# Optimization experiments

Hardware: AMD Instinct MI355X
Metric: run time of the kernel (lower is better)

The kernel has to match this reference:

```python
import jax, jax.numpy as jnp
import numpy as np
from jax import lax

# Hyperparameters from unifiedloss(__init__ defaults / init_kwargs)
WEIGHT = 1.0
DELTA = 0.6
GAMMA = 0.5
LABEL_SMOOTHING = 0.1
OUT_CHANNELS = 2
ALPHA = 0.9  # border_uncertainty inner-border weight
BETA = 0.9   # border_uncertainty outer-border weight
EPS = 1e-7


def _morph_3x3(x, is_dilate):
    # Binary morphology with a 3x3 ones structuring element == max/min pool.
    # x: [B, C, H, W]. 'SAME' padding with the reduction identity matches
    # ignoring out-of-image pixels.
    if is_dilate:
        return lax.reduce_window(x, -jnp.inf, lax.max, (1, 1, 3, 3), (1, 1, 1, 1), 'SAME')
    return lax.reduce_window(x, jnp.inf, lax.min, (1, 1, 3, 3), (1, 1, 1, 1), 'SAME')


def setup_inputs() -> dict:
    key = jax.random.key(0)
    k1, k2 = jax.random.split(key)
    B, C, H, W = 8, 2, 1024, 1024
    pred = jax.random.normal(k1, (B, C, H, W), dtype=jnp.float32)
    # one-hot binary ground truth (channel 0 = background, channel 1 = foreground)
    labels = jax.random.randint(k2, (B, H, W), 0, 2)
    target = jax.nn.one_hot(labels, C, dtype=jnp.float32).transpose(0, 3, 1, 2)
    return {"pred": pred, "target": target}


def reference(pred, target):
    # --- boundary uncertainty (vectorized over batch; all-zero samples give
    # erode = dilate = 0 so res = 0, matching the original early-return) ---
    im_erode = _morph_3x3(target, False)
    im_dilate = _morph_3x3(target, True)
    t = ALPHA * (target - im_erode) + BETA * (im_dilate - target) + im_erode

    # --- label smoothing ---
    t = t * (1.0 - LABEL_SMOOTHING) + LABEL_SMOOTHING / OUT_CHANNELS

    # --- valid-pixel mask: channel sum == 1 (only clean one-hot pixels kept) ---
    mf = (jnp.sum(t, axis=1) == 1.0).astype(pred.dtype)  # [B, H, W]
    n = jnp.sum(mf)

    p = jnp.clip(jax.nn.sigmoid(pred), EPS, 1.0 - EPS)  # [B, C, H, W]

    # --- asymmetric focal Tversky loss (masked per-class sums) ---
    tp = jnp.einsum('bhw,bchw->c', mf, t * p)
    fn = jnp.einsum('bhw,bchw->c', mf, t * (1.0 - p))
    fp = jnp.einsum('bhw,bchw->c', mf, (1.0 - t) * p)
    dice = (tp + EPS) / (tp + DELTA * fn + (1.0 - DELTA) * fp + EPS)
    back_dice = 1.0 - dice[0]
    fore_dice = (1.0 - dice[1]) * (1.0 - dice[1]) ** (-GAMMA)
    ftl = (back_dice + fore_dice) * 0.5

    # --- asymmetric focal loss (masked mean over pixels) ---
    ce = -t * jnp.log(p)  # [B, C, H, W]
    back_ce = (1.0 - DELTA) * (1.0 - p[:, 0]) ** GAMMA * ce[:, 0]
    fore_ce = DELTA * ce[:, 1]
    fl = jnp.sum(mf * (back_ce + fore_ce)) / n

    return WEIGHT * ftl + (1.0 - WEIGHT) * fl
```

## Files before the change

kernel.cpp:

```cpp
#include <hip/hip_runtime.h>
#include <math.h>

#define HH 1024
#define WW 1024
#define NB 8
#define ROWS 8
#define SW 256
#define STRIPES (WW / SW)
#define CHUNKS (HH / ROWS)
#define WPB (STRIPES * CHUNKS)
#define TOTAL_WAVES (NB * WPB)
#define NBLK (TOTAL_WAVES / 4)

__global__ __launch_bounds__(256) void ul_main(const float* __restrict__ pred,
                                               const float* __restrict__ target,
                                               float* __restrict__ partials) {
    const int wv   = threadIdx.x >> 6;
    const int lane = threadIdx.x & 63;
    const int wid  = (blockIdx.x << 2) | wv;
    const int b      = wid >> 9;
    const int rem    = wid & 511;
    const int stripe = rem & 3;
    const int chunk  = rem >> 2;
    const int c0     = stripe * SW;
    const int r0     = chunk * ROWS;
    const int col4   = c0 + lane * 4;

    const float* __restrict__ t1p = target + (size_t)(2 * b + 1) * (HH * WW);
    const float* __restrict__ p0p = pred   + (size_t)(2 * b)     * (HH * WW);
    const float* __restrict__ p1p = p0p + (size_t)HH * WW;

    const int excL = (c0 > 0) ? (c0 - 1) : 0;
    const int excR = (c0 + SW < WW) ? (c0 + SW) : (WW - 1);
    const int exc  = (lane == 0) ? excL : excR;

    float4 vm[ROWS + 2];
    unsigned ebPack = 0;
    #pragma unroll
    for (int i = 0; i < ROWS + 2; ++i) {
        int h = r0 - 1 + i;
        h = h < 0 ? 0 : (h >= HH ? HH - 1 : h);
        const float* rp = t1p + (size_t)h * WW;
        vm[i] = *(const float4*)(rp + col4);
        float ev = (lane < 2) ? rp[exc] : 0.0f;
        ebPack |= (ev > 0.5f ? 1u : 0u) << i;
    }
    const unsigned ebR = __shfl(ebPack, 1);

    unsigned pbits[ROWS + 2], w6[ROWS + 2];
    #pragma unroll
    for (int i = 0; i < ROWS + 2; ++i) {
        unsigned p = (vm[i].x > 0.5f ? 1u : 0u) | (vm[i].y > 0.5f ? 2u : 0u) |
                     (vm[i].z > 0.5f ? 4u : 0u) | (vm[i].w > 0.5f ? 8u : 0u);
        pbits[i] = p;
        const unsigned pl = __shfl_up(p, 1);
        const unsigned pr = __shfl_down(p, 1);
        const unsigned lb = (lane == 0)  ? ((ebPack >> i) & 1u) : ((pl >> 3) & 1u);
        const unsigned rb = (lane == 63) ? ((ebR    >> i) & 1u) : (pr & 1u);
        w6[i] = lb | (p << 1) | (rb << 5);
    }

    unsigned unis[ROWS];
    #pragma unroll
    for (int j = 0; j < ROWS; ++j) {
        const unsigned A = w6[j] & w6[j + 1] & w6[j + 2];
        const unsigned O = w6[j] | w6[j + 1] | w6[j + 2];
        const unsigned all1 = A & (A >> 1) & (A >> 2);
        const unsigned any1 = O | (O >> 1) | (O >> 2);
        unis[j] = (all1 | ~any1) & 0xFu;
    }

    float4 x0[ROWS], x1[ROWS];
    #pragma unroll
    for (int j = 0; j < ROWS; ++j) {
        if (unis[j]) {
            const size_t off = (size_t)(r0 + j) * WW + col4;
            x0[j] = *(const float4*)(p0p + off);
            x1[j] = *(const float4*)(p1p + off);
        }
    }

    float s_p0 = 0.f, s_lp0 = 0.f, s_p1 = 0.f, s_lp1 = 0.f;
    int nC = 0, nL = 0;
    #pragma unroll
    for (int j = 0; j < ROWS; ++j) {
        const unsigned uni = unis[j];
        if (uni) {
            const unsigned lb4 = pbits[j + 1];
            nC += __popc(uni);
            nL += __popc(uni & lb4);
            #define UL_DO_K(K, C0, C1)                                          \
                if ((uni >> K) & 1u) {                                          \
                    float sg0 = 1.0f / (1.0f + expf(-(C0)));                    \
                    float sg1 = 1.0f / (1.0f + expf(-(C1)));                    \
                    sg0 = fminf(fmaxf(sg0, 1e-7f), 1.0f - 1e-7f);               \
                    sg1 = fminf(fmaxf(sg1, 1e-7f), 1.0f - 1e-7f);               \
                    s_p0 += sg0; s_p1 += sg1;                                   \
                    if ((lb4 >> K) & 1u) { s_lp0 += sg0; s_lp1 += sg1; }        \
                }
            UL_DO_K(0, x0[j].x, x1[j].x)
            UL_DO_K(1, x0[j].y, x1[j].y)
            UL_DO_K(2, x0[j].z, x1[j].z)
            UL_DO_K(3, x0[j].w, x1[j].w)
            #undef UL_DO_K
        }
    }

    #pragma unroll
    for (int off = 32; off; off >>= 1) {
        s_p0  += __shfl_xor(s_p0,  off, 64);
        s_lp0 += __shfl_xor(s_lp0, off, 64);
        s_p1  += __shfl_xor(s_p1,  off, 64);
        s_lp1 += __shfl_xor(s_lp1, off, 64);
        nC    += __shfl_xor(nC,    off, 64);
        nL    += __shfl_xor(nL,    off, 64);
    }

    __shared__ float sm[4][6];
    if (lane == 0) {
        sm[wv][0] = s_p0;  sm[wv][1] = s_lp0;
        sm[wv][2] = s_p1;  sm[wv][3] = s_lp1;
        sm[wv][4] = (float)nC; sm[wv][5] = (float)nL;
    }
    __syncthreads();
    if (threadIdx.x < 8) {
        const int k = threadIdx.x;
        const float v = (k < 6) ? (sm[0][k] + sm[1][k] + sm[2][k] + sm[3][k]) : 0.0f;
        partials[(size_t)blockIdx.x * 8 + k] = v;
    }
}

__global__ __launch_bounds__(256) void ul_final(const float* __restrict__ ws,
                                                float* __restrict__ out) {
    const int t = threadIdx.x, lane = t & 63, wv = t >> 6;
    float a0 = 0.f, a1 = 0.f, a2 = 0.f, a3 = 0.f;
    #pragma unroll
    for (int r = 0; r < 8; ++r) {
        const float4 v = ((const float4*)ws)[t + 256 * r];
        a0 += v.x; a1 += v.y; a2 += v.z; a3 += v.w;
    }
    #pragma unroll
    for (int off = 32; off >= 2; off >>= 1) {
        a0 += __shfl_xor(a0, off, 64); a1 += __shfl_xor(a1, off, 64);
        a2 += __shfl_xor(a2, off, 64); a3 += __shfl_xor(a3, off, 64);
    }
    __shared__ float sm[4][2][4];
    if (lane < 2) {
        sm[wv][lane][0] = a0; sm[wv][lane][1] = a1;
        sm[wv][lane][2] = a2; sm[wv][lane][3] = a3;
    }
    __syncthreads();
    if (t == 0) {
        float Sp0 = 0.f, SLp0 = 0.f, Sp1 = 0.f, SLp1 = 0.f, N = 0.f, NL = 0.f;
        #pragma unroll
        for (int w = 0; w < 4; ++w) {
            Sp0 += sm[w][0][0]; SLp0 += sm[w][0][1];
            Sp1 += sm[w][0][2]; SLp1 += sm[w][0][3];
            N   += sm[w][1][0]; NL   += sm[w][1][1];
        }
        const float tp0 = 0.95f * Sp0 - 0.9f * SLp0;
        const float st0 = 0.95f * N   - 0.9f * NL;
        const float fn0 = st0 - tp0;
        const float fp0 = Sp0 - tp0;
        const float tp1 = 0.05f * Sp1 + 0.9f * SLp1;
        const float st1 = 0.05f * N   + 0.9f * NL;
        const float fn1 = st1 - tp1;
        const float fp1 = Sp1 - tp1;
        const float d0 = (tp0 + 1e-7f) / (tp0 + 0.6f * fn0 + 0.4f * fp0 + 1e-7f);
        const float d1 = (tp1 + 1e-7f) / (tp1 + 0.6f * fn1 + 0.4f * fp1 + 1e-7f);
        const float back = 1.0f - d0;
        const float fore = sqrtf(fmaxf(1.0f - d1, 0.0f));
        out[0] = 0.5f * (back + fore);
    }
}

extern "C" void kernel_launch(void* const* d_in, const int* in_sizes, int n_in,
                              void* d_out, int out_size, void* d_ws, size_t ws_size,
                              hipStream_t stream) {
    const float* pred   = (const float*)d_in[0];
    const float* target = (const float*)d_in[1];
    float* partials = (float*)d_ws;
    float* out      = (float*)d_out;

    ul_main<<<NBLK, 256, 0, stream>>>(pred, target, partials);
    ul_final<<<1, 256, 0, stream>>>(partials, out);
}
```

Before: 21.62 us.

## Share stripe-edge halo bits between waves via LDS instead of extra scalar loads

Each block now covers one full 8-row chunk across the entire width, with each of the 4 waves handling a 256-column stripe. Left and right halo column bits come from neighbouring waves through shared memory, replacing the per-row scalar edge loads. Bit masks are packed into 64-bit and 32-bit registers to reduce register use, and launch_bounds requests 4 blocks per CU. The cost is an added __syncthreads before the pred loads can be issued.

```diff
diff --git a/kernel.cpp b/kernel.cpp
--- a/kernel.cpp
+++ b/kernel.cpp
@@ -5,75 +5,73 @@
 #define WW 1024
 #define NB 8
 #define ROWS 8
-#define SW 256
-#define STRIPES (WW / SW)
 #define CHUNKS (HH / ROWS)
-#define WPB (STRIPES * CHUNKS)
-#define TOTAL_WAVES (NB * WPB)
-#define NBLK (TOTAL_WAVES / 4)
+#define NBLK (NB * CHUNKS)
 
-__global__ __launch_bounds__(256) void ul_main(const float* __restrict__ pred,
-                                               const float* __restrict__ target,
-                                               float* __restrict__ partials) {
+__global__ __launch_bounds__(256, 4) void ul_main(const float* __restrict__ pred,
+                                                  const float* __restrict__ target,
+                                                  float* __restrict__ partials) {
     const int wv   = threadIdx.x >> 6;
     const int lane = threadIdx.x & 63;
-    const int wid  = (blockIdx.x << 2) | wv;
-    const int b      = wid >> 9;
-    const int rem    = wid & 511;
-    const int stripe = rem & 3;
-    const int chunk  = rem >> 2;
-    const int c0     = stripe * SW;
-    const int r0     = chunk * ROWS;
-    const int col4   = c0 + lane * 4;
+    const int b     = blockIdx.x >> 7;
+    const int chunk = blockIdx.x & 127;
+    const int r0    = chunk * ROWS;
+    const int col4  = wv * 256 + lane * 4;
 
     const float* __restrict__ t1p = target + (size_t)(2 * b + 1) * (HH * WW);
     const float* __restrict__ p0p = pred   + (size_t)(2 * b)     * (HH * WW);
-    const float* __restrict__ p1p = p0p + (size_t)HH * WW;
-
-    const int excL = (c0 > 0) ? (c0 - 1) : 0;
-    const int excR = (c0 + SW < WW) ? (c0 + SW) : (WW - 1);
-    const int exc  = (lane == 0) ? excL : excR;
+    const float* __restrict__ p1p = p0p + (size_t)(HH * WW);
 
     float4 vm[ROWS + 2];
-    unsigned ebPack = 0;
     #pragma unroll
     for (int i = 0; i < ROWS + 2; ++i) {
         int h = r0 - 1 + i;
         h = h < 0 ? 0 : (h >= HH ? HH - 1 : h);
-        const float* rp = t1p + (size_t)h * WW;
-        vm[i] = *(const float4*)(rp + col4);
-        float ev = (lane < 2) ? rp[exc] : 0.0f;
-        ebPack |= (ev > 0.5f ? 1u : 0u) << i;
+        vm[i] = *(const float4*)(t1p + (size_t)h * WW + col4);
     }
-    const unsigned ebR = __shfl(ebPack, 1);
 
-    unsigned pbits[ROWS + 2], w6[ROWS + 2];
+    unsigned long long ppack = 0;
+    unsigned plpack = 0, prpack = 0, myL = 0, myR = 0;
     #pragma unroll
     for (int i = 0; i < ROWS + 2; ++i) {
-        unsigned p = (vm[i].x > 0.5f ? 1u : 0u) | (vm[i].y > 0.5f ? 2u : 0u) |
-                     (vm[i].z > 0.5f ? 4u : 0u) | (vm[i].w > 0.5f ? 8u : 0u);
-        pbits[i] = p;
-        const unsigned pl = __shfl_up(p, 1);
-        const unsigned pr = __shfl_down(p, 1);
-        const unsigned lb = (lane == 0)  ? ((ebPack >> i) & 1u) : ((pl >> 3) & 1u);
-        const unsigned rb = (lane == 63) ? ((ebR    >> i) & 1u) : (pr & 1u);
+        const unsigned p = (vm[i].x > 0.5f ? 1u : 0u) | (vm[i].y > 0.5f ? 2u : 0u) |
+                           (vm[i].z > 0.5f ? 4u : 0u) | (vm[i].w > 0.5f ? 8u : 0u);
+        ppack |= (unsigned long long)p << (4 * i);
+        myL   |= (p & 1u) << i;
+        myR   |= ((p >> 3) & 1u) << i;
+        plpack |= (((__shfl_up(p, 1) >> 3) & 1u)) << i;
+        prpack |= ((__shfl_down(p, 1) & 1u)) << i;
+    }
+
+    __shared__ unsigned eL[4], eR[4];
+    const unsigned lbm = __shfl(myL, 0);
+    const unsigned rbm = __shfl(myR, 63);
+    if (lane == 0) { eL[wv] = lbm; eR[wv] = rbm; }
+    __syncthreads();
+    const unsigned Lh = (wv > 0) ? eR[wv - 1] : lbm;
+    const unsigned Rh = (wv < 3) ? eL[wv + 1] : rbm;
+
+    unsigned w6[ROWS + 2];
+    #pragma unroll
+    for (int i = 0; i < ROWS + 2; ++i) {
+        const unsigned p  = (unsigned)(ppack >> (4 * i)) & 0xFu;
+        const unsigned lb = (lane == 0)  ? ((Lh >> i) & 1u) : ((plpack >> i) & 1u);
+        const unsigned rb = (lane == 63) ? ((Rh >> i) & 1u) : ((prpack >> i) & 1u);
         w6[i] = lb | (p << 1) | (rb << 5);
     }
-
-    unsigned unis[ROWS];
+    unsigned unis = 0;
     #pragma unroll
     for (int j = 0; j < ROWS; ++j) {
         const unsigned A = w6[j] & w6[j + 1] & w6[j + 2];
         const unsigned O = w6[j] | w6[j + 1] | w6[j + 2];
-        const unsigned all1 = A & (A >> 1) & (A >> 2);
-        const unsigned any1 = O | (O >> 1) | (O >> 2);
-        unis[j] = (all1 | ~any1) & 0xFu;
+        const unsigned u4 = ((A & (A >> 1) & (A >> 2)) | ~(O | (O >> 1) | (O >> 2))) & 0xFu;
+        unis |= u4 << (4 * j);
     }
 
     float4 x0[ROWS], x1[ROWS];
     #pragma unroll
     for (int j = 0; j < ROWS; ++j) {
-        if (unis[j]) {
+        if ((unis >> (4 * j)) & 0xFu) {
             const size_t off = (size_t)(r0 + j) * WW + col4;
             x0[j] = *(const float4*)(p0p + off);
             x1[j] = *(const float4*)(p1p + off);
@@ -84,9 +82,9 @@
     int nC = 0, nL = 0;
     #pragma unroll
     for (int j = 0; j < ROWS; ++j) {
-        const unsigned uni = unis[j];
+        const unsigned uni = (unis >> (4 * j)) & 0xFu;
         if (uni) {
-            const unsigned lb4 = pbits[j + 1];
+            const unsigned lb4 = (unsigned)(ppack >> (4 * (j + 1))) & 0xFu;
             nC += __popc(uni);
             nL += __popc(uni & lb4);
             #define UL_DO_K(K, C0, C1)                                          \
```

Result: faster. 20.91 us (-3.3%).
